# Kernel optimization log

Hardware: AMD Instinct MI355X
Metric: run time of the kernel (lower is better)

## Reference

```python
import jax, jax.numpy as jnp
import numpy as np

N = 100000
E = 1600000
NEG_SLOPE = 0.2

def _gat_layer(x, src, dst, W, a_s, a_d, b, n):
    # GATConv (heads=1): h = xW; alpha_ij = softmax_i(leaky_relu(a_s.h_j + a_d.h_i))
    h = x @ W                                   # [N, F]
    s_src = h @ a_s                             # [N]
    s_dst = h @ a_d                             # [N]
    logits = jax.nn.leaky_relu(s_src[src] + s_dst[dst], NEG_SLOPE)  # [E]
    m = jax.ops.segment_max(logits, dst, num_segments=n)
    m = jnp.where(jnp.isfinite(m), m, 0.0)
    w = jnp.exp(logits - m[dst])
    denom = jax.ops.segment_sum(w, dst, num_segments=n)
    alpha = w / (denom[dst] + 1e-16)            # neighbor softmax per target node
    out = jax.ops.segment_sum(alpha[:, None] * h[src], dst, num_segments=n)
    return out + b

def setup_inputs() -> dict:
    key = jax.random.key(0)
    ks = jax.random.split(key, 12)
    def glorot(k, shape):
        fan = shape[0] + shape[-1] if len(shape) > 1 else shape[0]
        return jax.random.normal(k, shape, jnp.float32) * jnp.sqrt(2.0 / fan)
    x = jax.random.normal(ks[0], (N, 128), jnp.float32)
    edge_index = jax.random.randint(ks[1], (2, E), 0, N, dtype=jnp.int32)
    return {
        'x': x, 'edge_index': edge_index,
        'W1': glorot(ks[2], (128, 64)), 'a1s': glorot(ks[3], (64,)), 'a1d': glorot(ks[4], (64,)), 'b1': jnp.zeros((64,), jnp.float32),
        'W2': glorot(ks[5], (64, 64)), 'a2s': glorot(ks[6], (64,)), 'a2d': glorot(ks[7], (64,)), 'b2': jnp.zeros((64,), jnp.float32),
        'W3': glorot(ks[8], (64, 32)), 'a3s': glorot(ks[9], (32,)), 'a3d': glorot(ks[10], (32,)), 'b3': jnp.zeros((32,), jnp.float32),
    }

def reference(x, edge_index, W1, a1s, a1d, b1, W2, a2s, a2d, b2, W3, a3s, a3d, b3):
    n = x.shape[0]
    # PyG GATConv adds self-loops by default
    loops = jnp.arange(n, dtype=edge_index.dtype)
    src = jnp.concatenate([edge_index[0], loops])
    dst = jnp.concatenate([edge_index[1], loops])
    h = _gat_layer(x, src, dst, W1, a1s, a1d, b1, n)
    h = jax.nn.relu(h)  # dropout is identity in eval mode
    h = _gat_layer(h, src, dst, W2, a2s, a2d, b2, n)
    h = jax.nn.relu(h)
    h = _gat_layer(h, src, dst, W3, a3s, a3d, b3, n)
    return jax.nn.log_softmax(h, axis=1)
```

## Files before the change

kernel.cpp:

```cpp
#include <hip/hip_runtime.h>
#include <cstddef>
#include <cstdint>

#define NEG_SLOPE 0.2f

__device__ __forceinline__ unsigned short f2bf(float f) {
    unsigned int u = __float_as_uint(f);
    u = (u + 0x7fff + ((u >> 16) & 1)) >> 16;
    return (unsigned short)u;
}
__device__ __forceinline__ float bf_lo(unsigned int u) { return __uint_as_float(u << 16); }
__device__ __forceinline__ float bf_hi(unsigned int u) { return __uint_as_float(u & 0xffff0000u); }

typedef __attribute__((ext_vector_type(8))) short bf16x8;
typedef __attribute__((ext_vector_type(4))) float f32x4;
typedef __attribute__((ext_vector_type(2))) float f32x2;


constexpr int BIN_BLOCKS = 256;
constexpr int MAX_NBK = 1024;

__global__ __launch_bounds__(256) void zero_k(int* __restrict__ p, int n) {
    int i = blockIdx.x * blockDim.x + threadIdx.x;
    if (i < n) p[i] = 0;
}

__global__ __launch_bounds__(256) void bin_hist_k(const int* __restrict__ dst, int E,
                                                  int* __restrict__ btot,
                                                  int* __restrict__ blkoff,
                                                  int nbk, int chunk) {
    __shared__ int hist[MAX_NBK];
    for (int i = threadIdx.x; i < nbk; i += 256) hist[i] = 0;
    __syncthreads();
    const int lo = blockIdx.x * chunk;
    const int hi = min(lo + chunk, E);
    for (int e = lo + threadIdx.x; e < hi; e += 256)
        atomicAdd(&hist[dst[e] >> 7], 1);
    __syncthreads();
    const int B = gridDim.x;
    for (int i = threadIdx.x; i < nbk; i += 256)
        blkoff[i * B + blockIdx.x] = atomicAdd(&btot[i], hist[i]);
}

__global__ __launch_bounds__(256) void scan_small_k(const int* __restrict__ btot,
                                                    int* __restrict__ obk, int nbk) {
    __shared__ int sh[MAX_NBK];
    const int tid = threadIdx.x;
    for (int i = tid; i < nbk; i += 256) sh[i] = btot[i];
    __syncthreads();
    if (tid < 64) {
        int run = 0;
        for (int b0 = 0; b0 < nbk; b0 += 64) {
            const int i = b0 + tid;
            int v = (i < nbk) ? sh[i] : 0;
            int inc = v;
#pragma unroll
            for (int o = 1; o < 64; o <<= 1) {
                int u = __shfl_up(inc, o);
                if (tid >= o) inc += u;
            }
            if (i < nbk) sh[i] = run + inc - v;
            run += __shfl(inc, 63);
        }
        if (tid == 0) obk[nbk] = run;
    }
    __syncthreads();
    for (int i = tid; i < nbk; i += 256) obk[i] = sh[i];
}

__global__ __launch_bounds__(256) void bin_scatter_k(const int* __restrict__ ei, int E,
                                                     const int* __restrict__ obk,
                                                     const int* __restrict__ blkoff,
                                                     int* __restrict__ eb, int nbk,
                                                     int chunk) {
    __shared__ int cur[MAX_NBK];
    __shared__ int off_s[MAX_NBK];
    const int B = gridDim.x;
    for (int i = threadIdx.x; i < nbk; i += 256) {
        cur[i] = 0;
        off_s[i] = obk[i] + blkoff[i * B + blockIdx.x];
    }
    __syncthreads();
    const int lo = blockIdx.x * chunk;
    const int hi = min(lo + chunk, E);
    for (int e = lo + threadIdx.x; e < hi; e += 256) {
        int s = ei[e];
        int d = ei[E + e];
        int b = d >> 7;
        int idx = atomicAdd(&cur[b], 1);
        eb[off_s[b] + idx] = (s << 7) | (d & 127);
    }
}

__global__ __launch_bounds__(256) void bucket_build_k(const int* __restrict__ eb,
                                                      const int* __restrict__ obk,
                                                      int* __restrict__ row_ptr,
                                                      int* __restrict__ col,
                                                      int n, int nbk) {
    __shared__ int c[128];
    __shared__ int rp[128];
    const int b = blockIdx.x;
    const int t = threadIdx.x;
    const int beg = obk[b];
    const int end = obk[b + 1];
    const int bbase = beg + b * 128;
    if (t < 128) c[t] = 1;
    __syncthreads();
    for (int i = beg + t; i < end; i += 256)
        atomicAdd(&c[eb[i] & 127], 1);
    __syncthreads();
    if (t < 64) {
        int v0 = c[2 * t], v1 = c[2 * t + 1];
        int pair = v0 + v1;
        int inc = pair;
        for (int o = 1; o < 64; o <<= 1) {
            int u = __shfl_up(inc, o);
            if (t >= o) inc += u;
        }
        int ex = inc - pair;
        rp[2 * t] = bbase + ex;
        rp[2 * t + 1] = bbase + ex + v0;
    }
    __syncthreads();
    const int node = b * 128 + t;
    if (t < 128 && node < n) {
        row_ptr[node] = rp[t];
        col[rp[t]] = node;
    }
    if (b == 0 && t == 0) row_ptr[n] = obk[nbk] + n;
    __syncthreads();
    if (t < 128) c[t] = 1;
    __syncthreads();
    for (int i = beg + t; i < end; i += 256) {
        int p = eb[i];
        int dl = p & 127;
        int idx = atomicAdd(&c[dl], 1);
        col[rp[dl] + idx] = p >> 7;
    }
}


template <int K, int F>
__launch_bounds__(256)
__global__ void gemm_mfma_k(const float* __restrict__ x, const float* __restrict__ W,
                            const float* __restrict__ a_s, const float* __restrict__ a_d,
                            unsigned short* __restrict__ hb, float* __restrict__ ss,
                            float* __restrict__ sd, int n) {
    constexpr int MT = 64;
    constexpr int KP = K + 8;
    constexpr int NT = F / 16;
    constexpr int KC = K / 32;

    __shared__ unsigned short xb[MT * KP];
    __shared__ unsigned short wb[F * KP];

    const int tid = threadIdx.x;
    const int lane = tid & 63;
    const int wv = tid >> 6;
    const int base = blockIdx.x * MT;

    for (int i = tid; i < MT * K / 4; i += 256) {
        int row = i / (K / 4);
        int c4 = i % (K / 4);
        float4 v = make_float4(0.f, 0.f, 0.f, 0.f);
        if (base + row < n)
            v = *(const float4*)&x[(size_t)(base + row) * K + 4 * c4];
        ushort4 b;
        b.x = f2bf(v.x); b.y = f2bf(v.y); b.z = f2bf(v.z); b.w = f2bf(v.w);
        *(ushort4*)&xb[row * KP + 4 * c4] = b;
    }
    for (int i = tid; i < K * F / 4; i += 256) {
        int nn = i % F;
        int k4 = i / F;
        ushort4 b;
        b.x = f2bf(W[(size_t)(4 * k4 + 0) * F + nn]);
        b.y = f2bf(W[(size_t)(4 * k4 + 1) * F + nn]);
        b.z = f2bf(W[(size_t)(4 * k4 + 2) * F + nn]);
        b.w = f2bf(W[(size_t)(4 * k4 + 3) * F + nn]);
        *(ushort4*)&wb[nn * KP + 4 * k4] = b;
    }
    __syncthreads();

    const int mrow = lane & 15;
    const int quad = lane >> 4;

    f32x4 acc[NT];
#pragma unroll
    for (int t = 0; t < NT; ++t) acc[t] = (f32x4){0.f, 0.f, 0.f, 0.f};

#pragma unroll
    for (int kc = 0; kc < KC; ++kc) {
        const int kof = kc * 32 + quad * 8;
        bf16x8 af = *(const bf16x8*)&xb[(wv * 16 + mrow) * KP + kof];
#pragma unroll
        for (int t = 0; t < NT; ++t) {
            bf16x8 bfr = *(const bf16x8*)&wb[(t * 16 + mrow) * KP + kof];
            acc[t] = __builtin_amdgcn_mfma_f32_16x16x32_bf16(af, bfr, acc[t], 0, 0, 0);
        }
    }

    float as_c[NT], ad_c[NT];
#pragma unroll
    for (int t = 0; t < NT; ++t) { as_c[t] = a_s[t * 16 + mrow]; ad_c[t] = a_d[t * 16 + mrow]; }

#pragma unroll
    for (int r = 0; r < 4; ++r) {
        const int node = base + wv * 16 + quad * 4 + r;
        float ps = 0.f, pd = 0.f;
#pragma unroll
        for (int t = 0; t < NT; ++t) {
            ps = fmaf(acc[t][r], as_c[t], ps);
            pd = fmaf(acc[t][r], ad_c[t], pd);
        }
#pragma unroll
        for (int o = 1; o < 16; o <<= 1) {
            ps += __shfl_xor(ps, o);
            pd += __shfl_xor(pd, o);
        }
        if (node < n) {
#pragma unroll
            for (int t = 0; t < NT; ++t)
                hb[(size_t)node * F + t * 16 + mrow] = f2bf(acc[t][r]);
            if (mrow == 0) { ss[node] = ps; sd[node] = pd; }
        }
    }
}


template <int K, int F>
__launch_bounds__(512)
__global__ void agg_gemm_k(const int* __restrict__ row_ptr, const int* __restrict__ col,
                           const unsigned short* __restrict__ hbi,
                           const float* __restrict__ ssi, const float* __restrict__ sdi,
                           const float* __restrict__ bias,
                           const float* __restrict__ W,
                           const float* __restrict__ a_s, const float* __restrict__ a_d,
                           unsigned short* __restrict__ hbo, float* __restrict__ sso,
                           float* __restrict__ sdo, int n) {
    static_assert(K == 64, "agg phase assumes 64 input channels");
    constexpr int S = 8;
    constexpr int MT = 64;
    constexpr int KP = K + 8;
    constexpr int NT = F / 16;
    constexpr int KC = K / 32;

    __shared__ unsigned short xb[MT * KP];
    __shared__ unsigned short wb[F * KP];

    const int tid = threadIdx.x;
    const int lane = tid & 63;
    const int wv = tid >> 6;
    const int base = blockIdx.x * MT;

    for (int i = tid; i < K * F / 4; i += 512) {
        int nn = i % F;
        int k4 = i / F;
        ushort4 b;
        b.x = f2bf(W[(size_t)(4 * k4 + 0) * F + nn]);
        b.y = f2bf(W[(size_t)(4 * k4 + 1) * F + nn]);
        b.z = f2bf(W[(size_t)(4 * k4 + 2) * F + nn]);
        b.w = f2bf(W[(size_t)(4 * k4 + 3) * F + nn]);
        *(ushort4*)&wb[nn * KP + 4 * k4] = b;
    }

    const int ls = lane & (S - 1);
    const int lbase = lane - ls;
    const int nl = tid >> 3;
    const int node = base + nl;

    float val[8] = {0.f, 0.f, 0.f, 0.f, 0.f, 0.f, 0.f, 0.f};
    if (node < n) {
        const int beg = row_ptr[node];
        const int end = row_ptr[node + 1];
        const float sdv = sdi[node];
        float z0 = ssi[node] + sdv;
        z0 = (z0 > 0.f) ? z0 : NEG_SLOPE * z0;

        float s = 0.f;
        f32x2 acc2[4];
#pragma unroll
        for (int i = 0; i < 4; ++i) acc2[i] = (f32x2){0.f, 0.f};

        for (int b0 = beg; b0 < end; b0 += S) {
            const int j = b0 + ls;
            int   c = 0;
            float logit = -__builtin_inff();
            if (j < end) {
                c = col[j];
                float z = ssi[c] + sdv;
                logit = (z > 0.f) ? z : NEG_SLOPE * z;
            }
            const float w = __expf(logit - z0);
            s += w;
            const unsigned int pk = ((unsigned int)f2bf(w) << 17) | (unsigned int)c;

            auto gather = [&](int tt) {
                const unsigned int pe = __shfl(pk, lbase + tt);
                const int ct = (int)(pe & 0x1ffffu);
                const float wt = __uint_as_float((pe >> 17) << 16);
                const uint4 hv = *(const uint4*)&hbi[(size_t)ct * K + 8 * ls];
                f32x2 p;
                p.x = bf_lo(hv.x); p.y = bf_hi(hv.x); acc2[0] += p * wt;
                p.x = bf_lo(hv.y); p.y = bf_hi(hv.y); acc2[1] += p * wt;
                p.x = bf_lo(hv.z); p.y = bf_hi(hv.z); acc2[2] += p * wt;
                p.x = bf_lo(hv.w); p.y = bf_hi(hv.w); acc2[3] += p * wt;
            };

            const int cnt = min(S, end - b0);
            int t = 0;
            for (; t + 3 < cnt; t += 4) {
                gather(t); gather(t + 1); gather(t + 2); gather(t + 3);
            }
            for (; t < cnt; ++t) gather(t);
        }
#pragma unroll
        for (int o = S / 2; o; o >>= 1) s += __shfl_xor(s, o);
        const float inv = 1.f / (s + 1e-16f);
        val[0] = acc2[0].x; val[1] = acc2[0].y; val[2] = acc2[1].x; val[3] = acc2[1].y;
        val[4] = acc2[2].x; val[5] = acc2[2].y; val[6] = acc2[3].x; val[7] = acc2[3].y;
#pragma unroll
        for (int i = 0; i < 8; ++i)
            val[i] = fmaxf(val[i] * inv + bias[8 * ls + i], 0.f);
    }
    {
        ushort4 p0, p1;
        p0.x = f2bf(val[0]); p0.y = f2bf(val[1]); p0.z = f2bf(val[2]); p0.w = f2bf(val[3]);
        p1.x = f2bf(val[4]); p1.y = f2bf(val[5]); p1.z = f2bf(val[6]); p1.w = f2bf(val[7]);
        *(ushort4*)&xb[nl * KP + 8 * ls] = p0;
        *(ushort4*)&xb[nl * KP + 8 * ls + 4] = p1;
    }

    __syncthreads();

    if (wv < 4) {
        const int mrow = lane & 15;
        const int quad = lane >> 4;

        f32x4 acc[NT];
#pragma unroll
        for (int t = 0; t < NT; ++t) acc[t] = (f32x4){0.f, 0.f, 0.f, 0.f};

#pragma unroll
        for (int kc = 0; kc < KC; ++kc) {
            const int kof = kc * 32 + quad * 8;
            bf16x8 af = *(const bf16x8*)&xb[(wv * 16 + mrow) * KP + kof];
#pragma unroll
            for (int t = 0; t < NT; ++t) {
                bf16x8 bfr = *(const bf16x8*)&wb[(t * 16 + mrow) * KP + kof];
                acc[t] = __builtin_amdgcn_mfma_f32_16x16x32_bf16(af, bfr, acc[t], 0, 0, 0);
            }
        }

        float as_c[NT], ad_c[NT];
#pragma unroll
        for (int t = 0; t < NT; ++t) { as_c[t] = a_s[t * 16 + mrow]; ad_c[t] = a_d[t * 16 + mrow]; }

#pragma unroll
        for (int r = 0; r < 4; ++r) {
            const int node2 = base + wv * 16 + quad * 4 + r;
            float ps = 0.f, pd = 0.f;
#pragma unroll
            for (int t = 0; t < NT; ++t) {
                ps = fmaf(acc[t][r], as_c[t], ps);
                pd = fmaf(acc[t][r], ad_c[t], pd);
            }
#pragma unroll
            for (int o = 1; o < 16; o <<= 1) {
                ps += __shfl_xor(ps, o);
                pd += __shfl_xor(pd, o);
            }
            if (node2 < n) {
#pragma unroll
                for (int t = 0; t < NT; ++t)
                    hbo[(size_t)node2 * F + t * 16 + mrow] = f2bf(acc[t][r]);
                if (mrow == 0) { sso[node2] = ps; sdo[node2] = pd; }
            }
        }
    }
}


template <int F, int S, bool RELU, bool LOGSM, bool OUTB>
__launch_bounds__(256)
__global__ void gat_agg_k(const int* __restrict__ row_ptr, const int* __restrict__ col,
                          const unsigned short* __restrict__ hb,
                          const float* __restrict__ ss, const float* __restrict__ sd,
                          const float* __restrict__ bias,
                          void* __restrict__ outv, int n) {
    constexpr int NPW = 64 / S;
    constexpr int NL = F / 8;
    constexpr int Q = S / NL;
    const int lane = threadIdx.x & 63;
    const int ls   = lane % S;
    const int q    = ls / NL;
    const int cl   = ls % NL;
    const int lbase = lane - ls;
    const int wave = (blockIdx.x * blockDim.x + threadIdx.x) >> 6;
    const int node = wave * NPW + lane / S;
    if (node >= n) return;

    const int beg = row_ptr[node];
    const int end = row_ptr[node + 1];
    const float sdv = sd[node];
    float z0 = ss[node] + sdv;
    z0 = (z0 > 0.f) ? z0 : NEG_SLOPE * z0;

    float s = 0.f;
    f32x2 acc2[4];
#pragma unroll
    for (int i = 0; i < 4; ++i) acc2[i] = (f32x2){0.f, 0.f};

    for (int base = beg; base < end; base += S) {
        const int j = base + ls;
        int   c = 0;
        float logit = -__builtin_inff();
        if (j < end) {
            c = col[j];
            float z = ss[c] + sdv;
            logit = (z > 0.f) ? z : NEG_SLOPE * z;
        }
        const float w = __expf(logit - z0);
        s += w;
        const unsigned int pk = ((unsigned int)f2bf(w) << 17) | (unsigned int)c;

        auto gather = [&](int tt) {
            const unsigned int pe = __shfl(pk, lbase + Q * tt + q);
            const int ct = (int)(pe & 0x1ffffu);
            const float wt = __uint_as_float((pe >> 17) << 16);
            const uint4 hv = *(const uint4*)&hb[(size_t)ct * F + 8 * cl];
            f32x2 p;
            p.x = bf_lo(hv.x); p.y = bf_hi(hv.x); acc2[0] += p * wt;
            p.x = bf_lo(hv.y); p.y = bf_hi(hv.y); acc2[1] += p * wt;
            p.x = bf_lo(hv.z); p.y = bf_hi(hv.z); acc2[2] += p * wt;
            p.x = bf_lo(hv.w); p.y = bf_hi(hv.w); acc2[3] += p * wt;
        };

        const int cnt = min(S, end - base);
        int t = 0;
        for (; Q * (t + 3) < cnt; t += 4) {
            gather(t); gather(t + 1); gather(t + 2); gather(t + 3);
        }
        for (; Q * (t + 1) < cnt; t += 2) { gather(t); gather(t + 1); }
        if (Q * t < cnt) gather(t);
    }

#pragma unroll
    for (int o = S / 2; o; o >>= 1) s += __shfl_xor(s, o);
    float val[8] = {acc2[0].x, acc2[0].y, acc2[1].x, acc2[1].y,
                    acc2[2].x, acc2[2].y, acc2[3].x, acc2[3].y};
#pragma unroll
    for (int o = NL; o < S; o <<= 1) {
#pragma unroll
        for (int i = 0; i < 8; ++i) val[i] += __shfl_xor(val[i], o);
    }

    const float inv = 1.f / (s + 1e-16f);
#pragma unroll
    for (int i = 0; i < 8; ++i) {
        val[i] = val[i] * inv + bias[8 * cl + i];
        if (RELU) val[i] = fmaxf(val[i], 0.f);
    }
    if (LOGSM) {
        float lm = val[0];
#pragma unroll
        for (int i = 1; i < 8; ++i) lm = fmaxf(lm, val[i]);
#pragma unroll
        for (int o = 1; o < NL; o <<= 1) lm = fmaxf(lm, __shfl_xor(lm, o));
        float ex = 0.f;
#pragma unroll
        for (int i = 0; i < 8; ++i) ex += __expf(val[i] - lm);
#pragma unroll
        for (int o = 1; o < NL; o <<= 1) ex += __shfl_xor(ex, o);
        const float lse = lm + __logf(ex);
#pragma unroll
        for (int i = 0; i < 8; ++i) val[i] -= lse;
    }
    if (q == 0) {
        if (OUTB) {
            unsigned short* out = (unsigned short*)outv;
            ushort4 p0, p1;
            p0.x = f2bf(val[0]); p0.y = f2bf(val[1]); p0.z = f2bf(val[2]); p0.w = f2bf(val[3]);
            p1.x = f2bf(val[4]); p1.y = f2bf(val[5]); p1.z = f2bf(val[6]); p1.w = f2bf(val[7]);
            *(ushort4*)&out[(size_t)node * F + 8 * cl] = p0;
            *(ushort4*)&out[(size_t)node * F + 8 * cl + 4] = p1;
        } else {
            float* out = (float*)outv;
            float4 v0 = make_float4(val[0], val[1], val[2], val[3]);
            float4 v1 = make_float4(val[4], val[5], val[6], val[7]);
            *(float4*)&out[(size_t)node * F + 8 * cl] = v0;
            *(float4*)&out[(size_t)node * F + 8 * cl + 4] = v1;
        }
    }
}


extern "C" void kernel_launch(void* const* d_in, const int* in_sizes, int n_in,
                              void* d_out, int out_size, void* d_ws, size_t ws_size,
                              hipStream_t stream) {
    const float* x  = (const float*)d_in[0];
    const int*   ei = (const int*)d_in[1];
    const float* W1 = (const float*)d_in[2];
    const float* a1s = (const float*)d_in[3];
    const float* a1d = (const float*)d_in[4];
    const float* b1  = (const float*)d_in[5];
    const float* W2 = (const float*)d_in[6];
    const float* a2s = (const float*)d_in[7];
    const float* a2d = (const float*)d_in[8];
    const float* b2  = (const float*)d_in[9];
    const float* W3 = (const float*)d_in[10];
    const float* a3s = (const float*)d_in[11];
    const float* a3d = (const float*)d_in[12];
    const float* b3  = (const float*)d_in[13];

    const int N = in_sizes[0] / 128;
    const int E = in_sizes[1] / 2;
    const int NBK = (N + 127) / 128;
    const int B = BIN_BLOCKS;

    char* wp = (char*)d_ws;
    auto alloc = [&](size_t bytes) -> void* {
        void* p = wp;
        wp += (bytes + 255) & ~(size_t)255;
        return p;
    };
    int* row_ptr = (int*)alloc((size_t)(N + 1) * 4);
    int* col     = (int*)alloc((size_t)(E + N) * 4);
    unsigned short* hb1 = (unsigned short*)alloc((size_t)N * 64 * 2);
    unsigned short* hb2 = (unsigned short*)alloc((size_t)N * 64 * 2);
    unsigned short* hb3 = (unsigned short*)alloc((size_t)N * 32 * 2);
    float* ss1 = (float*)alloc((size_t)N * 4);
    float* sd1 = (float*)alloc((size_t)N * 4);
    float* ss2 = (float*)alloc((size_t)N * 4);
    float* sd2 = (float*)alloc((size_t)N * 4);
    float* ss3 = (float*)alloc((size_t)N * 4);
    float* sd3 = (float*)alloc((size_t)N * 4);
    int* btot   = (int*)alloc((size_t)NBK * 4);
    int* blkoff = (int*)alloc((size_t)NBK * B * 4);
    int* obk    = (int*)alloc((size_t)(NBK + 1) * 4);
    int* eb     = (int*)alloc((size_t)E * 4);

    const int chunk = (E + B - 1) / B;

    zero_k<<<(NBK + 255) / 256, 256, 0, stream>>>(btot, NBK);
    bin_hist_k<<<B, 256, 0, stream>>>(ei + E, E, btot, blkoff, NBK, chunk);
    scan_small_k<<<1, 256, 0, stream>>>(btot, obk, NBK);
    bin_scatter_k<<<B, 256, 0, stream>>>(ei, E, obk, blkoff, eb, NBK, chunk);
    bucket_build_k<<<NBK, 256, 0, stream>>>(eb, obk, row_ptr, col, N, NBK);

    const int GB = (N + 63) / 64;

    gemm_mfma_k<128, 64><<<GB, 256, 0, stream>>>(x, W1, a1s, a1d, hb1, ss1, sd1, N);
    agg_gemm_k<64, 64><<<GB, 512, 0, stream>>>(row_ptr, col, hb1, ss1, sd1, b1,
                                               W2, a2s, a2d, hb2, ss2, sd2, N);
    agg_gemm_k<64, 32><<<GB, 512, 0, stream>>>(row_ptr, col, hb2, ss2, sd2, b2,
                                               W3, a3s, a3d, hb3, ss3, sd3, N);
    gat_agg_k<32, 16, false, true, false><<<(N + 15) / 16, 256, 0, stream>>>(
        row_ptr, col, hb3, ss3, sd3, b3, d_out, N);
}
```

Before: 288.6 us.

## Precompute per-edge attention weights in a separate edge pass before aggregation

Measured after the change: 322.3 us. +11.7%, slower.

```diff
diff --git a/kernel.cpp b/kernel.cpp
--- a/kernel.cpp
+++ b/kernel.cpp
@@ -96,6 +96,7 @@
                                                       const int* __restrict__ obk,
                                                       int* __restrict__ row_ptr,
                                                       int* __restrict__ col,
+                                                      int* __restrict__ edst,
                                                       int n, int nbk) {
     __shared__ int c[128];
     __shared__ int rp[128];
@@ -126,6 +127,7 @@
     if (t < 128 && node < n) {
         row_ptr[node] = rp[t];
         col[rp[t]] = node;
+        edst[rp[t]] = node;
     }
     if (b == 0 && t == 0) row_ptr[n] = obk[nbk] + n;
     __syncthreads();
@@ -135,8 +137,30 @@
         int p = eb[i];
         int dl = p & 127;
         int idx = atomicAdd(&c[dl], 1);
-        col[rp[dl] + idx] = p >> 7;
-    }
+        const int slot = rp[dl] + idx;
+        col[slot] = p >> 7;
+        edst[slot] = b * 128 + dl;
+    }
+}
+
+
+__global__ __launch_bounds__(256) void edge_w_k(const int* __restrict__ col,
+                                                const int* __restrict__ edst,
+                                                const float2* __restrict__ ssd,
+                                                int2* __restrict__ ew, int EN) {
+    const int e = blockIdx.x * blockDim.x + threadIdx.x;
+    if (e >= EN) return;
+    const int c = col[e];
+    const int d = edst[e];
+    const float2 pc = ssd[c];
+    const float2 pd = ssd[d];
+    float zs = pd.x + pd.y;
+    zs = (zs > 0.f) ? zs : NEG_SLOPE * zs;
+    float z = pc.x + pd.y;
+    z = (z > 0.f) ? z : NEG_SLOPE * z;
+    const float w = __expf(z - zs);
+    ew[e] = make_int2((int)(((unsigned int)f2bf(w) << 17) | (unsigned int)c),
+                      __float_as_int(w));
 }
 
 
@@ -144,8 +168,8 @@
 __launch_bounds__(256)
 __global__ void gemm_mfma_k(const float* __restrict__ x, const float* __restrict__ W,
                             const float* __restrict__ a_s, const float* __restrict__ a_d,
-                            unsigned short* __restrict__ hb, float* __restrict__ ss,
-                            float* __restrict__ sd, int n) {
+                            unsigned short* __restrict__ hb, float2* __restrict__ ssd,
+                            int n) {
     constexpr int MT = 64;
     constexpr int KP = K + 8;
     constexpr int NT = F / 16;
@@ -221,7 +245,7 @@
 #pragma unroll
             for (int t = 0; t < NT; ++t)
                 hb[(size_t)node * F + t * 16 + mrow] = f2bf(acc[t][r]);
-            if (mrow == 0) { ss[node] = ps; sd[node] = pd; }
+            if (mrow == 0) ssd[node] = make_float2(ps, pd);
         }
     }
 }
@@ -229,14 +253,14 @@
 
 template <int K, int F>
 __launch_bounds__(512)
-__global__ void agg_gemm_k(const int* __restrict__ row_ptr, const int* __restrict__ col,
+__global__ void agg_gemm_k(const int* __restrict__ row_ptr,
+                           const int2* __restrict__ ew,
                            const unsigned short* __restrict__ hbi,
-                           const float* __restrict__ ssi, const float* __restrict__ sdi,
                            const float* __restrict__ bias,
                            const float* __restrict__ W,
                            const float* __restrict__ a_s, const float* __restrict__ a_d,
-                           unsigned short* __restrict__ hbo, float* __restrict__ sso,
-                           float* __restrict__ sdo, int n) {
+                           unsigned short* __restrict__ hbo, float2* __restrict__ ssdo,
+                           int n) {
     static_assert(K == 64, "agg phase assumes 64 input channels");
     constexpr int S = 8;
     constexpr int MT = 64;
@@ -272,30 +296,22 @@
     if (node < n) {
         const int beg = row_ptr[node];
         const int end = row_ptr[node + 1];
-        const float sdv = sdi[node];
-        float z0 = ssi[node] + sdv;
-        z0 = (z0 > 0.f) ? z0 : NEG_SLOPE * z0;
 
         float s = 0.f;
         f32x2 acc2[4];
 #pragma unroll
         for (int i = 0; i < 4; ++i) acc2[i] = (f32x2){0.f, 0.f};
 
+        int2 nxt = (beg + ls < end) ? ew[beg + ls] : make_int2(0, 0);
         for (int b0 = beg; b0 < end; b0 += S) {
-            const int j = b0 + ls;
-            int   c = 0;
-            float logit = -__builtin_inff();
-            if (j < end) {
-                c = col[j];
-                float z = ssi[c] + sdv;
-                logit = (z > 0.f) ? z : NEG_SLOPE * z;
-            }
-            const float w = __expf(logit - z0);
-            s += w;
-            const unsigned int pk = ((unsigned int)f2bf(w) << 17) | (unsigned int)c;
+            const int2 cur = nxt;
+            const int jn = b0 + S + ls;
+            nxt = (jn < end) ? ew[jn] : make_int2(0, 0);
+            s += __int_as_float(cur.y);
+            const unsigned int pk = (unsigned int)cur.x;
 
             auto gather = [&](int tt) {
-                const unsigned int pe = __shfl(pk, lbase + tt);
+                const unsigned int pe = (unsigned int)__shfl((int)pk, lbase + tt);
                 const int ct = (int)(pe & 0x1ffffu);
                 const float wt = __uint_as_float((pe >> 17) << 16);
                 const uint4 hv = *(const uint4*)&hbi[(size_t)ct * K + 8 * ls];
@@ -307,11 +323,14 @@
             };
 
             const int cnt = min(S, end - b0);
-            int t = 0;
-            for (; t + 3 < cnt; t += 4) {
-                gather(t); gather(t + 1); gather(t + 2); gather(t + 3);
+            if (cnt == S) {
+                gather(0); gather(1); gather(2); gather(3);
+                gather(4); gather(5); gather(6); gather(7);
+            } else {
+                int t = 0;
+                for (; t + 1 < cnt; t += 2) { gather(t); gather(t + 1); }
+                if (t < cnt) gather(t);
             }
-            for (; t < cnt; ++t) gather(t);
         }
 #pragma unroll
         for (int o = S / 2; o; o >>= 1) s += __shfl_xor(s, o);
@@ -373,20 +392,20 @@
 #pragma unroll
                 for (int t = 0; t < NT; ++t)
                     hbo[(size_t)node2 * F + t * 16 + mrow] = f2bf(acc[t][r]);
-                if (mrow == 0) { sso[node2] = ps; sdo[node2] = pd; }
+                if (mrow == 0) ssdo[node2] = make_float2(ps, pd);
             }
         }
     }
 }
 
 
-template <int F, int S, bool RELU, bool LOGSM, bool OUTB>
+template <int F, int S>
 __launch_bounds__(256)
-__global__ void gat_agg_k(const int* __restrict__ row_ptr, const int* __restrict__ col,
+__global__ void gat_agg_k(const int* __restrict__ row_ptr,
+                          const int2* __restrict__ ew,
                           const unsigned short* __restrict__ hb,
-                          const float* __restrict__ ss, const float* __restrict__ sd,
                           const float* __restrict__ bias,
-                          void* __restrict__ outv, int n) {
+                          float* __restrict__ out, int n) {
     constexpr int NPW = 64 / S;
     constexpr int NL = F / 8;
     constexpr int Q = S / NL;
@@ -401,30 +420,22 @@
 
     const int beg = row_ptr[node];
     const int end = row_ptr[node + 1];
-    const float sdv = sd[node];
-    float z0 = ss[node] + sdv;
-    z0 = (z0 > 0.f) ? z0 : NEG_SLOPE * z0;
 
     float s = 0.f;
     f32x2 acc2[4];
 #pragma unroll
     for (int i = 0; i < 4; ++i) acc2[i] = (f32x2){0.f, 0.f};
 
-    for (int base = beg; base < end; base += S) {
-        const int j = base + ls;
-        int   c = 0;
-        float logit = -__builtin_inff();
-        if (j < end) {
-            c = col[j];
-            float z = ss[c] + sdv;
-            logit = (z > 0.f) ? z : NEG_SLOPE * z;
-        }
-        const float w = __expf(logit - z0);
-        s += w;
-        const unsigned int pk = ((unsigned int)f2bf(w) << 17) | (unsigned int)c;
+    int2 nxt = (beg + ls < end) ? ew[beg + ls] : make_int2(0, 0);
+    for (int b0 = beg; b0 < end; b0 += S) {
+        const int2 cur = nxt;
+        const int jn = b0 + S + ls;
+        nxt = (jn < end) ? ew[jn] : make_int2(0, 0);
+        s += __int_as_float(cur.y);
+        const unsigned int pk = (unsigned int)cur.x;
 
         auto gather = [&](int tt) {
-            const unsigned int pe = __shfl(pk, lbase + Q * tt + q);
+            const unsigned int pe = (unsigned int)__shfl((int)pk, lbase + Q * tt + q);
             const int ct = (int)(pe & 0x1ffffu);
             const float wt = __uint_as_float((pe >> 17) << 16);
             const uint4 hv = *(const uint4*)&hb[(size_t)ct * F + 8 * cl];
@@ -435,13 +446,15 @@
             p.x = bf_lo(hv.w); p.y = bf_hi(hv.w); acc2[3] += p * wt;
         };
 
-        const int cnt = min(S, end - base);
-        int t = 0;
-        for (; Q * (t + 3) < cnt; t += 4) {
-            gather(t); gather(t + 1); gather(t + 2); gather(t + 3);
-        }
-        for (; Q * (t + 1) < cnt; t += 2) { gather(t); gather(t + 1); }
-        if (Q * t < cnt) gather(t);
+        const int cnt = min(S, end - b0);
+        if (cnt == S) {
+#pragma unroll
+            for (int t = 0; t < S / Q; ++t) gather(t);
+        } else {
+            int t = 0;
+            for (; Q * (t + 1) < cnt; t += 2) { gather(t); gather(t + 1); }
+            if (Q * t < cnt) gather(t);
+        }
     }
 
 #pragma unroll
@@ -456,40 +469,28 @@
 
     const float inv = 1.f / (s + 1e-16f);
 #pragma unroll
-    for (int i = 0; i < 8; ++i) {
+    for (int i = 0; i < 8; ++i)
         val[i] = val[i] * inv + bias[8 * cl + i];
-        if (RELU) val[i] = fmaxf(val[i], 0.f);
-    }
-    if (LOGSM) {
-        float lm = val[0];
-#pragma unroll
-        for (int i = 1; i < 8; ++i) lm = fmaxf(lm, val[i]);
-#pragma unroll
-        for (int o = 1; o < NL; o <<= 1) lm = fmaxf(lm, __shfl_xor(lm, o));
-        float ex = 0.f;
-#pragma unroll
-        for (int i = 0; i < 8; ++i) ex += __expf(val[i] - lm);
-#pragma unroll
-        for (int o = 1; o < NL; o <<= 1) ex += __shfl_xor(ex, o);
-        const float lse = lm + __logf(ex);
-#pragma unroll
-        for (int i = 0; i < 8; ++i) val[i] -= lse;
-    }
+
+    float lm = val[0];
+#pragma unroll
+    for (int i = 1; i < 8; ++i) lm = fmaxf(lm, val[i]);
+#pragma unroll
+    for (int o = 1; o < NL; o <<= 1) lm = fmaxf(lm, __shfl_xor(lm, o));
+    float ex = 0.f;
+#pragma unroll
+    for (int i = 0; i < 8; ++i) ex += __expf(val[i] - lm);
+#pragma unroll
+    for (int o = 1; o < NL; o <<= 1) ex += __shfl_xor(ex, o);
+    const float lse = lm + __logf(ex);
+#pragma unroll
+    for (int i = 0; i < 8; ++i) val[i] -= lse;
+
     if (q == 0) {
-        if (OUTB) {
-            unsigned short* out = (unsigned short*)outv;
-            ushort4 p0, p1;
-            p0.x = f2bf(val[0]); p0.y = f2bf(val[1]); p0.z = f2bf(val[2]); p0.w = f2bf(val[3]);
-            p1.x = f2bf(val[4]); p1.y = f2bf(val[5]); p1.z = f2bf(val[6]); p1.w = f2bf(val[7]);
-            *(ushort4*)&out[(size_t)node * F + 8 * cl] = p0;
-            *(ushort4*)&out[(size_t)node * F + 8 * cl + 4] = p1;
-        } else {
-            float* out = (float*)outv;
-            float4 v0 = make_float4(val[0], val[1], val[2], val[3]);
-            float4 v1 = make_float4(val[4], val[5], val[6], val[7]);
-            *(float4*)&out[(size_t)node * F + 8 * cl] = v0;
-            *(float4*)&out[(size_t)node * F + 8 * cl + 4] = v1;
-        }
+        float4 v0 = make_float4(val[0], val[1], val[2], val[3]);
+        float4 v1 = make_float4(val[4], val[5], val[6], val[7]);
+        *(float4*)&out[(size_t)node * F + 8 * cl] = v0;
+        *(float4*)&out[(size_t)node * F + 8 * cl + 4] = v1;
     }
 }
 
@@ -514,6 +515,7 @@
 
     const int N = in_sizes[0] / 128;
     const int E = in_sizes[1] / 2;
+    const int EN = E + N;
     const int NBK = (N + 127) / 128;
     const int B = BIN_BLOCKS;
 
@@ -524,16 +526,15 @@
         return p;
     };
     int* row_ptr = (int*)alloc((size_t)(N + 1) * 4);
-    int* col     = (int*)alloc((size_t)(E + N) * 4);
+    int* col     = (int*)alloc((size_t)EN * 4);
+    int* edst    = (int*)alloc((size_t)EN * 4);
+    int2* ewb    = (int2*)alloc((size_t)EN * 8);
     unsigned short* hb1 = (unsigned short*)alloc((size_t)N * 64 * 2);
     unsigned short* hb2 = (unsigned short*)alloc((size_t)N * 64 * 2);
     unsigned short* hb3 = (unsigned short*)alloc((size_t)N * 32 * 2);
-    float* ss1 = (float*)alloc((size_t)N * 4);
-    float* sd1 = (float*)alloc((size_t)N * 4);
-    float* ss2 = (float*)alloc((size_t)N * 4);
-    float* sd2 = (float*)alloc((size_t)N * 4);
-    float* ss3 = (float*)alloc((size_t)N * 4);
-    float* sd3 = (float*)alloc((size_t)N * 4);
+    float2* ssd1 = (float2*)alloc((size_t)N * 8);
+    float2* ssd2 = (float2*)alloc((size_t)N * 8);
+    float2* ssd3 = (float2*)alloc((size_t)N * 8);
     int* btot   = (int*)alloc((size_t)NBK * 4);
     int* blkoff = (int*)alloc((size_t)NBK * B * 4);
     int* obk    = (int*)alloc((size_t)(NBK + 1) * 4);
@@ -545,15 +546,19 @@
     bin_hist_k<<<B, 256, 0, stream>>>(ei + E, E, btot, blkoff, NBK, chunk);
     scan_small_k<<<1, 256, 0, stream>>>(btot, obk, NBK);
     bin_scatter_k<<<B, 256, 0, stream>>>(ei, E, obk, blkoff, eb, NBK, chunk);
-    bucket_build_k<<<NBK, 256, 0, stream>>>(eb, obk, row_ptr, col, N, NBK);
+    bucket_build_k<<<NBK, 256, 0, stream>>>(eb, obk, row_ptr, col, edst, N, NBK);
 
     const int GB = (N + 63) / 64;
-
-    gemm_mfma_k<128, 64><<<GB, 256, 0, stream>>>(x, W1, a1s, a1d, hb1, ss1, sd1, N);
-    agg_gemm_k<64, 64><<<GB, 512, 0, stream>>>(row_ptr, col, hb1, ss1, sd1, b1,
-                                               W2, a2s, a2d, hb2, ss2, sd2, N);
-    agg_gemm_k<64, 32><<<GB, 512, 0, stream>>>(row_ptr, col, hb2, ss2, sd2, b2,
-                                               W3, a3s, a3d, hb3, ss3, sd3, N);
-    gat_agg_k<32, 16, false, true, false><<<(N + 15) / 16, 256, 0, stream>>>(
-        row_ptr, col, hb3, ss3, sd3, b3, d_out, N);
-}
+    const int GE = (EN + 255) / 256;
+
+    gemm_mfma_k<128, 64><<<GB, 256, 0, stream>>>(x, W1, a1s, a1d, hb1, ssd1, N);
+    edge_w_k<<<GE, 256, 0, stream>>>(col, edst, ssd1, ewb, EN);
+    agg_gemm_k<64, 64><<<GB, 512, 0, stream>>>(row_ptr, ewb, hb1, b1,
+                                               W2, a2s, a2d, hb2, ssd2, N);
+    edge_w_k<<<GE, 256, 0, stream>>>(col, edst, ssd2, ewb, EN);
+    agg_gemm_k<64, 32><<<GB, 512, 0, stream>>>(row_ptr, ewb, hb2, b2,
+                                               W3, a3s, a3d, hb3, ssd3, N);
+    edge_w_k<<<GE, 256, 0, stream>>>(col, edst, ssd3, ewb, EN);
+    gat_agg_k<32, 16><<<(N + 15) / 16, 256, 0, stream>>>(
+        row_ptr, ewb, hb3, b3, (float*)d_out, N);
+}
```
